# Kernel tuning notes

Measured on AMD Instinct MI355X. Metric: run time of the kernel, lower is better.

Reference implementation:

```python
import jax, jax.numpy as jnp
import numpy as np
from jax import lax

IMG_SIZE = 1024
NUM_CLASSES = 80
TOP_K = 300          # self.top_k
CLS_THRES = 0.05     # self.cls_thres
IOU_THR = 0.5        # nms overlap
BBOX_STD = jnp.array([0.1, 0.1, 0.2, 0.2], dtype=jnp.float32)


def make_anchors(img_size=IMG_SIZE):
    """Standard RetinaNet anchors: P3-P7, 3 ratios x 3 scales per cell."""
    strides = [8, 16, 32, 64, 128]
    ratios = np.array([0.5, 1.0, 2.0])
    scales = 2.0 ** (np.arange(3) / 3.0)
    out = []
    for s in strides:
        base = 4.0 * s
        ws, hs = [], []
        for r in ratios:
            for sc in scales:
                ws.append(base * sc / np.sqrt(r))
                hs.append(base * sc * np.sqrt(r))
        ws = np.array(ws); hs = np.array(hs)  # [9]
        fs = img_size // s
        shift = (np.arange(fs) + 0.5) * s
        cy, cx = np.meshgrid(shift, shift, indexing='ij')
        cx = cx.ravel()[:, None]; cy = cy.ravel()[:, None]
        a = np.stack([cx - ws / 2, cy - hs / 2, cx + ws / 2, cy + hs / 2], axis=-1)
        out.append(a.reshape(-1, 4))
    return np.concatenate(out, axis=0).astype(np.float32)  # [A,4]


def setup_inputs() -> dict:
    key = jax.random.key(0)
    k1, k2 = jax.random.split(key)
    anchors = jnp.asarray(make_anchors())[None]          # [1,A,4]
    A = anchors.shape[1]
    classifications = jax.random.uniform(k1, (1, A, NUM_CLASSES), dtype=jnp.float32)
    regressions = jax.random.normal(k2, (1, A, 4), dtype=jnp.float32)
    return {"classifications": classifications, "regressions": regressions,
            "anchors": anchors, "img_h": IMG_SIZE, "img_w": IMG_SIZE}


def decode_boxes(anchors, regressions):
    # BBoxTransform: mean=0, std=[.1,.1,.2,.2]
    w = anchors[..., 2] - anchors[..., 0]
    h = anchors[..., 3] - anchors[..., 1]
    cx = anchors[..., 0] + 0.5 * w
    cy = anchors[..., 1] + 0.5 * h
    d = regressions * BBOX_STD
    pcx = cx + d[..., 0] * w
    pcy = cy + d[..., 1] * h
    pw = jnp.exp(d[..., 2]) * w
    ph = jnp.exp(d[..., 3]) * h
    return jnp.stack([pcx - 0.5 * pw, pcy - 0.5 * ph,
                      pcx + 0.5 * pw, pcy + 0.5 * ph], axis=-1)


def pairwise_iou(b):  # b: [K,4]
    x1, y1, x2, y2 = b[:, 0], b[:, 1], b[:, 2], b[:, 3]
    area = jnp.clip(x2 - x1, 0) * jnp.clip(y2 - y1, 0)
    iw = jnp.clip(jnp.minimum(x2[:, None], x2[None]) - jnp.maximum(x1[:, None], x1[None]), 0)
    ih = jnp.clip(jnp.minimum(y2[:, None], y2[None]) - jnp.maximum(y1[:, None], y1[None]), 0)
    inter = iw * ih
    return inter / (area[:, None] + area[None] - inter + 1e-8)


def nms_one_class(boxes, scores_c):
    """Greedy NMS over top-K candidates above threshold for one class."""
    s = jnp.where(scores_c > CLS_THRES, scores_c, -jnp.inf)
    top_scores, top_idx = lax.top_k(s, TOP_K)        # sorted descending
    cand_valid = top_scores > CLS_THRES
    iou = pairwise_iou(boxes[top_idx])               # [K,K]
    idxs = jnp.arange(TOP_K)

    def body(suppressed, i):
        sup_i = suppressed[i] | (~cand_valid[i])
        new_sup = suppressed | ((~sup_i) & (iou[i] > IOU_THR) & (idxs > i))
        return new_sup, ~sup_i

    _, keep = lax.scan(body, jnp.zeros(TOP_K, bool), idxs)
    return top_idx, top_scores, keep


def reference(classifications, regressions, anchors, img_h, img_w):
    boxes = decode_boxes(anchors, regressions)       # [1,A,4]
    boxes = jnp.stack([jnp.maximum(boxes[..., 0], 0.0),
                       jnp.maximum(boxes[..., 1], 0.0),
                       jnp.minimum(boxes[..., 2], float(img_w)),
                       jnp.minimum(boxes[..., 3], float(img_h))], axis=-1)
    boxes0 = boxes[0]                                # [A,4]  (batch item 0, as original)
    cls0 = classifications[0]                        # [A,C]
    A, C = cls0.shape

    # per-class NMS, vmapped over the class axis
    top_idx, top_scores, keep = jax.vmap(nms_one_class, in_axes=(None, 1))(boxes0, cls0)
    # scatter kept scores back into dense [A,C] matrix (original 'scores' tensor)
    scores_mat = jnp.zeros((A, C), cls0.dtype).at[top_idx, jnp.arange(C)[:, None]].set(
        jnp.where(keep, top_scores, 0.0))

    scores_max = scores_mat.max(axis=1)
    labels = scores_mat.argmax(axis=1)
    valid = scores_max > 0
    # fixed-shape (jit-friendly) equivalent of the original's boolean filtering:
    final_scores = jnp.where(valid, scores_max, 0.0)
    final_labels = jnp.where(valid, labels, -1)
    final_boxes = jnp.where(valid[:, None], boxes0, 0.0)
    return final_scores, final_labels, final_boxes
```

## Files before the change

### kernel.cpp

```cpp
#include <hip/hip_runtime.h>
#include <cstdint>

typedef unsigned long long u64;
typedef unsigned int u32;

#define CLS_T    0.05f
#define T1G      0.997933f
#define TOPK     300
#define NWORDS   5
#define HBINS    2560
#define KEY_BASE 0x3D000000u
#define CCAP     512
#define NBLK     2048
#define SCAP     16
#define OVBIT    0x80000000u

__device__ inline u32 bin_of_bits(u32 bits) {
    u32 b = (bits - KEY_BASE) >> 14;
    if (b > (HBINS - 1)) b = HBINS - 1;
    return b;
}

__device__ inline float4 decode_box(const float* __restrict__ anc,
                                    const float* __restrict__ reg,
                                    u32 a, float W, float H)
{
    float x1 = anc[(size_t)a*4+0], y1 = anc[(size_t)a*4+1];
    float x2 = anc[(size_t)a*4+2], y2 = anc[(size_t)a*4+3];
    float w = x2 - x1, h = y2 - y1;
    float cx = x1 + 0.5f*w, cy = y1 + 0.5f*h;
    float r0 = reg[(size_t)a*4+0]*0.1f, r1 = reg[(size_t)a*4+1]*0.1f;
    float r2 = reg[(size_t)a*4+2]*0.2f, r3 = reg[(size_t)a*4+3]*0.2f;
    float pcx = cx + r0*w, pcy = cy + r1*h;
    float pw_ = expf(r2)*w, ph_ = expf(r3)*h;
    float4 b;
    b.x = fmaxf(pcx - 0.5f*pw_, 0.0f);
    b.y = fmaxf(pcy - 0.5f*ph_, 0.0f);
    b.z = fminf(pcx + 0.5f*pw_, W);
    b.w = fminf(pcy + 0.5f*ph_, H);
    return b;
}

__device__ inline void cex(u64& v, u64 p, bool lo, bool up) {
    u64 mx = v > p ? v : p;
    u64 mn = v > p ? p : v;
    v = (lo == up) ? mx : mn;
}
__device__ inline void s1(u64& v, u32 tid, u32 kk, u32 j) {
    u64 p = __shfl_xor((unsigned long long)v, (int)j, 64);
    cex(v, p, (tid & j) == 0, (tid & kk) == 0);
}
__device__ inline void l1(u64* sm, u64& v, u32 tid, u32 kk, u32 j) {
    __syncthreads();
    if (tid < 512) sm[tid] = v;
    __syncthreads();
    if (tid < 512) {
        u64 p = sm[tid ^ j];
        cex(v, p, (tid & j) == 0, (tid & kk) == 0);
    }
}

__global__ void decode_kernel(const float* __restrict__ anc,
                              const float* __restrict__ reg,
                              const int* __restrict__ ph,
                              const int* __restrict__ pw,
                              float* __restrict__ boxes,
                              u64* __restrict__ akey, int A)
{
    int a = blockIdx.x * blockDim.x + threadIdx.x;
    if (a >= A) return;
    akey[a] = 0;
    float W = (float)(*pw), H = (float)(*ph);
    float4 b = decode_box(anc, reg, (u32)a, W, H);
    boxes[a*4+0] = b.x; boxes[a*4+1] = b.y;
    boxes[a*4+2] = b.z; boxes[a*4+3] = b.w;
}

__global__ __launch_bounds__(256) void fused_scan_kernel(
    const float* __restrict__ cls,
    u64* __restrict__ akey,
    u64* __restrict__ gbuf, u32* __restrict__ segcnt, int A)
{
    const int tid = threadIdx.x;
    const int blk = blockIdx.x;

    for (int a = blk * 256 + tid; a < A; a += NBLK * 256) akey[a] = 0;

    __shared__ u32 cnt[80];
    __shared__ u64 buf[80][SCAP];
    __shared__ u32 s_over;
    for (int i = tid; i < 80; i += 256) cnt[i] = 0;
    if (tid == 0) s_over = 0;
    __syncthreads();

    size_t Nf4 = (size_t)A * 20;
    const size_t stride = (size_t)NBLK * 256;
    const float4* p4 = (const float4*)cls;
    for (size_t i = (size_t)blk * 256 + tid; i < Nf4; i += 2 * stride) {
        float4 v0 = p4[i];
        size_t i1 = i + stride;
        bool has1 = (i1 < Nf4);
        float4 v1;
        if (has1) v1 = p4[i1];
        {
            float ss[4] = {v0.x, v0.y, v0.z, v0.w};
            #pragma unroll
            for (int q = 0; q < 4; ++q) {
                if (ss[q] > T1G) {
                    u32 flat = (u32)(i * 4 + q);
                    u32 a = flat / 80u;
                    u32 c = flat - a * 80u;
                    u32 p = atomicAdd(&cnt[c], 1u);
                    if (p < SCAP) buf[c][p] = ((u64)__float_as_uint(ss[q]) << 32) | (u32)(~a);
                    else s_over = 1;
                }
            }
        }
        if (has1) {
            float ss[4] = {v1.x, v1.y, v1.z, v1.w};
            #pragma unroll
            for (int q = 0; q < 4; ++q) {
                if (ss[q] > T1G) {
                    u32 flat = (u32)(i1 * 4 + q);
                    u32 a = flat / 80u;
                    u32 c = flat - a * 80u;
                    u32 p = atomicAdd(&cnt[c], 1u);
                    if (p < SCAP) buf[c][p] = ((u64)__float_as_uint(ss[q]) << 32) | (u32)(~a);
                    else s_over = 1;
                }
            }
        }
    }
    __syncthreads();

    const u32 ob = s_over ? OVBIT : 0u;
    for (int m = tid; m < 80 * SCAP; m += 256) {
        int c = m / SCAP, e = m - c * SCAP;
        u32 cc = cnt[c]; if (cc > SCAP) cc = SCAP;
        if ((u32)e < cc)
            gbuf[((size_t)c * NBLK + blk) * SCAP + e] = buf[c][e];
    }
    for (int c = tid; c < 80; c += 256) {
        u32 cc = cnt[c]; if (cc > SCAP) cc = SCAP;
        segcnt[(size_t)c * NBLK + blk] = cc | ob;
    }
}

__global__ __launch_bounds__(640) void class_fused_kernel(
    const u32* __restrict__ segcnt, const u64* __restrict__ gbuf,
    const float* __restrict__ cls,
    const float* __restrict__ anc, const float* __restrict__ reg,
    const int* __restrict__ ph, const int* __restrict__ pw,
    u64* __restrict__ akey, int A, int C)
{
    const int c = blockIdx.x;
    const u32 tid = threadIdx.x;
    const int lane = tid & 63;

    __shared__ u32 sh[HBINS];
    __shared__ u32 sp[NBLK];
    __shared__ u64 cand[CCAP];
    __shared__ u32 wtot[8], wob[8];
    __shared__ u32 s_sel, s_cnt, s_rem;
    __shared__ float4 sbox[TOPK];
    __shared__ float  sbar[TOPK];
    __shared__ u64 iomaskT[NWORDS][TOPK];
    __shared__ u64 s_keep[NWORDS];

    const float W = (float)(*pw), H = (float)(*ph);

    u32 v4[4] = {0,0,0,0};
    u32 s = 0, ob = 0;
    if (tid < 512) {
        const u32* row = segcnt + (size_t)c * NBLK;
        #pragma unroll
        for (int q = 0; q < 4; ++q) {
            u32 r = row[tid * 4 + q];
            ob |= r & OVBIT;
            v4[q] = r & ~OVBIT;
            s += v4[q];
        }
    }
    u32 incl = s;
    #pragma unroll
    for (int d = 1; d < 64; d <<= 1) {
        u32 t = __shfl_up(incl, d, 64);
        if ((tid & 63) >= (u32)d) incl += t;
    }
    u64 obm = __ballot(ob != 0);
    if (tid < 512 && (tid & 63) == 63) {
        wtot[tid >> 6] = incl;
        wob [tid >> 6] = (obm != 0) ? 1u : 0u;
    }
    __syncthreads();
    u32 woff = 0, ntot = 0, obt = 0;
    #pragma unroll
    for (int w2 = 0; w2 < 8; ++w2) {
        u32 t = wtot[w2];
        obt |= wob[w2];
        if (w2 < (int)(tid >> 6)) woff += t;
        ntot += t;
    }
    if (tid < 512) {
        u32 base = woff + incl - s;
        #pragma unroll
        for (int q = 0; q < 4; ++q) { sp[tid * 4 + q] = base; base += v4[q]; }
    }
    __syncthreads();
    const u32 n = ntot;
    const bool over = (obt != 0);

    u32 cnt_f = 0;
    bool fast_ok = false;

    if (!over && n >= TOPK && n <= CCAP) {
        for (u32 i = tid; i < n; i += 640) {
            int lo = 0, hi = NBLK;
            while (hi - lo > 1) {
                int mid = (lo + hi) >> 1;
                if (sp[mid] <= i) lo = mid; else hi = mid;
            }
            u32 e = i - sp[lo];
            cand[i] = gbuf[((size_t)c * NBLK + lo) * SCAP + e];
        }
        cnt_f = n;
        fast_ok = true;
    }

    if (!fast_ok) {
        __syncthreads();
        for (int i = tid; i < HBINS; i += 640) sh[i] = 0;
        if (tid == 0) s_cnt = 0;
        __syncthreads();
        for (int a = tid; a < A; a += 640) {
            float sc = cls[(size_t)a * C + c];
            if (sc > CLS_T) atomicAdd(&sh[bin_of_bits(__float_as_uint(sc))], 1u);
        }
        __syncthreads();
        if (tid == 0) {
            u32 cum = 0; int sel = 0;
            for (int d = HBINS - 1; d >= 0; --d) {
                u32 nc = cum + sh[d];
                if (nc >= TOPK) { sel = d; break; }
                cum = nc;
            }
            s_sel = (u32)sel; s_rem = TOPK - cum;
        }
        __syncthreads();
        const u32 sel1 = s_sel;
        __syncthreads();
        for (int i = tid; i < 256; i += 640) sh[i] = 0;
        __syncthreads();
        for (int a = tid; a < A; a += 640) {
            float sc = cls[(size_t)a * C + c];
            if (sc > CLS_T) {
                u32 k = __float_as_uint(sc) - KEY_BASE;
                u32 b = k >> 14; if (b >= HBINS) b = HBINS - 1;
                if (b == sel1) atomicAdd(&sh[(k >> 6) & 0xFF], 1u);
            }
        }
        __syncthreads();
        if (tid == 0) {
            u32 rem = s_rem, cum = 0; int sel = 0;
            for (int d = 255; d >= 0; --d) {
                u32 nc = cum + sh[d];
                if (nc >= rem) { sel = d; break; }
                cum = nc;
            }
            s_sel = (sel1 << 14) | ((u32)sel << 6);
            s_cnt = 0;
        }
        __syncthreads();
        const u32 thresh = s_sel;
        for (int a = tid; a < A; a += 640) {
            float sc = cls[(size_t)a * C + c];
            if (sc > CLS_T) {
                u32 bits = __float_as_uint(sc);
                if (bits - KEY_BASE >= thresh) {
                    u32 p = atomicAdd(&s_cnt, 1u);
                    if (p < CCAP) cand[p] = ((u64)bits << 32) | (u32)(~(u32)a);
                }
            }
        }
        __syncthreads();
        cnt_f = s_cnt < CCAP ? s_cnt : CCAP;
    }

    for (u32 i = cnt_f + tid; i < CCAP; i += 640) cand[i] = 0;
    for (int m = tid; m < NWORDS * TOPK; m += 640) ((u64*)iomaskT)[m] = 0;
    __syncthreads();

    u64 v = 0;
    if (tid < 512) {
        v = cand[tid];
        for (u32 kk = 2; kk <= 64; kk <<= 1)
            for (u32 j = kk >> 1; j >= 1; j >>= 1)
                s1(v, tid, kk, j);
    }
    l1(cand, v, tid, 128u, 64u);
    if (tid < 512) for (u32 j = 32; j >= 1; j >>= 1) s1(v, tid, 128u, j);
    l1(cand, v, tid, 256u, 128u);
    l1(cand, v, tid, 256u, 64u);
    if (tid < 512) for (u32 j = 32; j >= 1; j >>= 1) s1(v, tid, 256u, j);
    l1(cand, v, tid, 512u, 256u);
    l1(cand, v, tid, 512u, 128u);
    l1(cand, v, tid, 512u, 64u);
    if (tid < 512) for (u32 j = 32; j >= 1; j >>= 1) s1(v, tid, 512u, j);

    const int T = (int)(cnt_f < TOPK ? cnt_f : TOPK);

    u64 key = v; u32 aidx = 0;
    if ((int)tid < T) {
        aidx = ~(u32)(key & 0xFFFFFFFFull);
        float4 b4 = decode_box(anc, reg, aidx, W, H);
        sbox[tid] = b4;
        sbar[tid] = fmaxf(b4.z - b4.x, 0.0f) * fmaxf(b4.w - b4.y, 0.0f);
    }
    __syncthreads();

    {
        const int jj = (int)(tid < 320 ? tid : tid - 320);
        const int p  = (int)(tid < 320 ? 0 : 1);
        if (jj < T) {
            float4 b = sbox[jj];
            float ar = sbar[jj];
            u64 cm[NWORDS] = {0,0,0,0,0};
            for (int i = p; i < jj; i += 2) {
                float4 bi = sbox[i];
                float iw = fmaxf(fminf(b.z, bi.z) - fmaxf(b.x, bi.x), 0.0f);
                float ih = fmaxf(fminf(b.w, bi.w) - fmaxf(b.y, bi.y), 0.0f);
                float inter = iw * ih;
                float uni = ((ar + sbar[i]) - inter) + 1e-8f;
                if (inter / uni > 0.5f) cm[i >> 6] |= 1ull << (i & 63);
            }
            #pragma unroll
            for (int w = 0; w < NWORDS; ++w)
                if (cm[w]) atomicOr(&iomaskT[w][jj], cm[w]);
        }
    }
    __syncthreads();

    if (tid < 64) {
        u64 K[NWORDS];
        #pragma unroll
        for (int w = 0; w < NWORDS; ++w) {
            int b = w * 64 + lane;
            bool valid = (b < T);
            u64 cmw = 0, se = 0;
            if (valid) {
                #pragma unroll
                for (int w2 = 0; w2 < NWORDS; ++w2)
                    if (w2 < w) se |= K[w2] & iomaskT[w2][b];
                cmw = iomaskT[w][b];
            }
            u64 U = __ballot(valid && se == 0);
            u64 Kw = 0;
            int guard = 0;
            while (U && guard++ < 64) {
                u64 newk = __ballot(((U >> lane) & 1ull) && ((cmw & U) == 0));
                Kw |= newk; U &= ~newk;
                u64 supp = __ballot((cmw & Kw) != 0);
                U &= ~supp;
            }
            K[w] = Kw;
        }
        if (lane == 0) {
            #pragma unroll
            for (int w = 0; w < NWORDS; ++w) s_keep[w] = K[w];
        }
    }
    __syncthreads();

    if ((int)tid < T) {
        if ((s_keep[tid >> 6] >> (tid & 63)) & 1ull) {
            u32 sbits = (u32)(key >> 32);
            u64 outk = ((u64)sbits << 32) | (u32)(255 - c);
            atomicMax(&akey[aidx], outk);
        }
    }
}

__global__ void finalize_kernel(const u64* __restrict__ akey,
                                const float* __restrict__ anc,
                                const float* __restrict__ reg,
                                const int* __restrict__ ph,
                                const int* __restrict__ pw,
                                float* __restrict__ out, int A)
{
    int a = blockIdx.x * blockDim.x + threadIdx.x;
    if (a >= A) return;
    float* scores = out;
    float* labels = out + A;
    float* boxes  = out + (size_t)2 * A;
    u64 k = akey[a];
    if (k) {
        scores[a] = __uint_as_float((u32)(k >> 32));
        labels[a] = (float)(int)(255u - (u32)(k & 0xFFFFFFFFull));
        float W = (float)(*pw), H = (float)(*ph);
        float4 b = decode_box(anc, reg, (u32)a, W, H);
        boxes[(size_t)a*4+0] = b.x; boxes[(size_t)a*4+1] = b.y;
        boxes[(size_t)a*4+2] = b.z; boxes[(size_t)a*4+3] = b.w;
    } else {
        scores[a] = 0.0f;
        labels[a] = -1.0f;
        boxes[(size_t)a*4+0] = 0.0f;
        boxes[(size_t)a*4+1] = 0.0f;
        boxes[(size_t)a*4+2] = 0.0f;
        boxes[(size_t)a*4+3] = 0.0f;
    }
}

__global__ void fb_finalize_kernel(const u64* __restrict__ akey,
                                   float* __restrict__ out, int A)
{
    int a = blockIdx.x * blockDim.x + threadIdx.x;
    if (a >= A) return;
    float* scores = out;
    float* labels = out + A;
    float* boxes  = out + (size_t)2 * A;
    u64 k = akey[a];
    if (k) {
        scores[a] = __uint_as_float((u32)(k >> 32));
        labels[a] = (float)(int)(255u - (u32)(k & 0xFFFFFFFFull));
    } else {
        scores[a] = 0.0f;
        labels[a] = -1.0f;
        boxes[(size_t)a*4+0] = 0.0f;
        boxes[(size_t)a*4+1] = 0.0f;
        boxes[(size_t)a*4+2] = 0.0f;
        boxes[(size_t)a*4+3] = 0.0f;
    }
}

#define FB_CAP 1024
__global__ __launch_bounds__(256) void fb_topk_nms_kernel(
    const float* __restrict__ cls,
    const float* __restrict__ boxes,
    u64* __restrict__ akey,
    int A, int C)
{
    const int c   = blockIdx.x;
    const int tid = threadIdx.x;

    __shared__ u32 hist[HBINS];
    __shared__ u64 cand[FB_CAP];
    __shared__ float bx1[TOPK], by1[TOPK], bx2[TOPK], by2[TOPK], bar[TOPK];
    __shared__ u64 iomask[TOPK][NWORDS];
    __shared__ u64 keepm[NWORDS];
    __shared__ u32 s_sel1, s_sel2, s_rem, s_cnt;

    for (int i = tid; i < HBINS; i += 256) hist[i] = 0;
    __syncthreads();
    for (int a = tid; a < A; a += 256) {
        float s = cls[(size_t)a * C + c];
        if (s > CLS_T) {
            u32 k = __float_as_uint(s) - KEY_BASE;
            u32 b = k >> 14; if (b >= HBINS) b = HBINS - 1;
            atomicAdd(&hist[b], 1u);
        }
    }
    __syncthreads();
    if (tid == 0) {
        u32 cum = 0; int sel = 0;
        for (int d = HBINS - 1; d >= 0; --d) {
            u32 nc = cum + hist[d];
            if (nc >= TOPK) { sel = d; break; }
            cum = nc;
        }
        s_sel1 = (u32)sel; s_rem = TOPK - cum;
    }
    __syncthreads();
    const u32 sel1 = s_sel1;

    for (int i = tid; i < 256; i += 256) hist[i] = 0;
    __syncthreads();
    for (int a = tid; a < A; a += 256) {
        float s = cls[(size_t)a * C + c];
        if (s > CLS_T) {
            u32 k = __float_as_uint(s) - KEY_BASE;
            u32 b = k >> 14; if (b >= HBINS) b = HBINS - 1;
            if (b == sel1) atomicAdd(&hist[(k >> 6) & 0xFF], 1u);
        }
    }
    __syncthreads();
    if (tid == 0) {
        u32 rem = s_rem, cum = 0; int sel = 0;
        for (int d = 255; d >= 0; --d) {
            u32 nc = cum + hist[d];
            if (nc >= rem) { sel = d; break; }
            cum = nc;
        }
        s_sel2 = (u32)sel; s_cnt = 0;
    }
    __syncthreads();
    const u32 thresh = (sel1 << 14) | (s_sel2 << 6);

    for (int a = tid; a < A; a += 256) {
        float s = cls[(size_t)a * C + c];
        if (s > CLS_T) {
            u32 bits = __float_as_uint(s);
            u32 k = bits - KEY_BASE;
            if (k >= thresh) {
                u32 pos = atomicAdd(&s_cnt, 1u);
                if (pos < FB_CAP) cand[pos] = ((u64)bits << 32) | (u32)(~(u32)a);
            }
        }
    }
    __syncthreads();
    const u32 total = s_cnt < FB_CAP ? s_cnt : FB_CAP;
    for (int i = tid; i < FB_CAP; i += 256)
        if (i >= (int)total) cand[i] = 0;
    __syncthreads();

    for (u32 kk = 2; kk <= FB_CAP; kk <<= 1) {
        for (u32 j = kk >> 1; j > 0; j >>= 1) {
            for (u32 i = tid; i < FB_CAP; i += 256) {
                u32 l = i ^ j;
                if (l > i) {
                    u64 av = cand[i], bv = cand[l];
                    bool up = ((i & kk) == 0);
                    if ((up && av < bv) || (!up && av > bv)) { cand[i] = bv; cand[l] = av; }
                }
            }
            __syncthreads();
        }
    }
    const int T = (int)(total < TOPK ? total : TOPK);

    for (int i = tid; i < T; i += 256) {
        u32 a = ~(u32)(cand[i] & 0xFFFFFFFFull);
        float x1 = boxes[(size_t)a*4+0], y1 = boxes[(size_t)a*4+1];
        float x2 = boxes[(size_t)a*4+2], y2 = boxes[(size_t)a*4+3];
        bx1[i] = x1; by1[i] = y1; bx2[i] = x2; by2[i] = y2;
        bar[i] = fmaxf(x2 - x1, 0.0f) * fmaxf(y2 - y1, 0.0f);
    }
    __syncthreads();

    for (int i = tid; i < T; i += 256) {
        u64 m[NWORDS] = {0,0,0,0,0};
        float x1 = bx1[i], y1 = by1[i], x2 = bx2[i], y2 = by2[i], ai = bar[i];
        for (int j = i + 1; j < T; ++j) {
            float iw = fmaxf(fminf(x2, bx2[j]) - fmaxf(x1, bx1[j]), 0.0f);
            float ih = fmaxf(fminf(y2, by2[j]) - fmaxf(y1, by1[j]), 0.0f);
            float inter = iw * ih;
            float uni = ((ai + bar[j]) - inter) + 1e-8f;
            if (inter / uni > 0.5f) m[j >> 6] |= 1ull << (j & 63);
        }
        for (int k2 = 0; k2 < NWORDS; ++k2) iomask[i][k2] = m[k2];
    }
    __syncthreads();

    if (tid == 0) {
        u64 sup[NWORDS] = {0,0,0,0,0};
        u64 kp [NWORDS] = {0,0,0,0,0};
        for (int i = 0; i < T; ++i) {
            if (!((sup[i >> 6] >> (i & 63)) & 1ull)) {
                kp[i >> 6] |= 1ull << (i & 63);
                for (int k2 = 0; k2 < NWORDS; ++k2) sup[k2] |= iomask[i][k2];
            }
        }
        for (int k2 = 0; k2 < NWORDS; ++k2) keepm[k2] = kp[k2];
    }
    __syncthreads();

    for (int i = tid; i < T; i += 256) {
        if ((keepm[i >> 6] >> (i & 63)) & 1ull) {
            u64 key = cand[i];
            u32 a = ~(u32)(key & 0xFFFFFFFFull);
            u32 sbits = (u32)(key >> 32);
            u64 outk = ((u64)sbits << 32) | (u32)(255 - c);
            atomicMax(&akey[a], outk);
        }
    }
}

extern "C" void kernel_launch(void* const* d_in, const int* in_sizes, int n_in,
                              void* d_out, int out_size, void* d_ws, size_t ws_size,
                              hipStream_t stream) {
    const float* cls = (const float*)d_in[0];
    const float* reg = (const float*)d_in[1];
    const float* anc = (const float*)d_in[2];
    const int*   ph  = (const int*)d_in[3];
    const int*   pw  = (const int*)d_in[4];

    int A = in_sizes[2] / 4;
    int C = in_sizes[0] / A;

    float* out       = (float*)d_out;
    float* out_boxes = out + (size_t)2 * A;

    size_t akey_bytes = (size_t)A * sizeof(u64);
    size_t off_sc     = (akey_bytes + 255) & ~(size_t)255;
    size_t sc_bytes   = (size_t)80 * NBLK * sizeof(u32);
    size_t off_gb     = (off_sc + sc_bytes + 255) & ~(size_t)255;
    size_t gb_bytes   = (size_t)80 * NBLK * SCAP * sizeof(u64);
    size_t need       = off_gb + gb_bytes;

    u64* akey = (u64*)d_ws;

    bool fastpath = (C == 80) && ((A & 3) == 0) && (A < (1 << 20)) && (ws_size >= need);

    if (fastpath) {
        u32* segcnt = (u32*)((char*)d_ws + off_sc);
        u64* gbuf   = (u64*)((char*)d_ws + off_gb);

        fused_scan_kernel<<<NBLK, 256, 0, stream>>>(cls, akey, gbuf, segcnt, A);
        class_fused_kernel<<<C, 640, 0, stream>>>(segcnt, gbuf, cls, anc, reg, ph, pw, akey, A, C);
        finalize_kernel<<<(A + 255) / 256, 256, 0, stream>>>(akey, anc, reg, ph, pw, out, A);
    } else {
        decode_kernel<<<(A + 255) / 256, 256, 0, stream>>>(anc, reg, ph, pw, out_boxes, akey, A);
        fb_topk_nms_kernel<<<C, 256, 0, stream>>>(cls, out_boxes, akey, A, C);
        fb_finalize_kernel<<<(A + 255) / 256, 256, 0, stream>>>(akey, out, A);
    }
}
```

Baseline: 52.21 us.

## Zero outputs in scan kernel and finalize only kept anchors via compact list

The output default fill (scores, labels, boxes) moves into the scan kernel's existing anchor loop. The class kernel now appends each kept anchor index to a global list through an atomic counter, and a light finalize kernel decodes boxes only for those entries instead of sweeping every anchor. Candidate gathering also changes from a per-element binary search to each thread copying its own segments directly. Duplicate anchors kept by several classes are written more than once with the same max key, and the direct copy adds serial per-thread loops.

```diff
diff --git a/kernel.cpp b/kernel.cpp
--- a/kernel.cpp
+++ b/kernel.cpp
@@ -14,6 +14,7 @@
 #define NBLK     2048
 #define SCAP     16
 #define OVBIT    0x80000000u
+#define KMAX     (80 * TOPK)
 
 __device__ inline u32 bin_of_bits(u32 bits) {
     u32 b = (bits - KEY_BASE) >> 14;
@@ -78,13 +79,25 @@
 
 __global__ __launch_bounds__(256) void fused_scan_kernel(
     const float* __restrict__ cls,
-    u64* __restrict__ akey,
-    u64* __restrict__ gbuf, u32* __restrict__ segcnt, int A)
+    u64* __restrict__ akey, float* __restrict__ out,
+    u64* __restrict__ gbuf, u32* __restrict__ segcnt,
+    u32* __restrict__ kcount, int A)
 {
     const int tid = threadIdx.x;
     const int blk = blockIdx.x;
 
-    for (int a = blk * 256 + tid; a < A; a += NBLK * 256) akey[a] = 0;
+    if (blk == 0 && tid == 0) *kcount = 0;
+
+    float* scores = out;
+    float* labels = out + A;
+    float4* boxes4 = (float4*)(out + (size_t)2 * A);
+    const float4 z4 = make_float4(0.f, 0.f, 0.f, 0.f);
+    for (int a = blk * 256 + tid; a < A; a += NBLK * 256) {
+        akey[a] = 0;
+        scores[a] = 0.0f;
+        labels[a] = -1.0f;
+        boxes4[a] = z4;
+    }
 
     __shared__ u32 cnt[80];
     __shared__ u64 buf[80][SCAP];
@@ -151,17 +164,17 @@
     const float* __restrict__ cls,
     const float* __restrict__ anc, const float* __restrict__ reg,
     const int* __restrict__ ph, const int* __restrict__ pw,
-    u64* __restrict__ akey, int A, int C)
+    u64* __restrict__ akey, u32* __restrict__ kcount, u32* __restrict__ klist,
+    int A, int C)
 {
     const int c = blockIdx.x;
     const u32 tid = threadIdx.x;
     const int lane = tid & 63;
 
     __shared__ u32 sh[HBINS];
-    __shared__ u32 sp[NBLK];
     __shared__ u64 cand[CCAP];
     __shared__ u32 wtot[8], wob[8];
-    __shared__ u32 s_sel, s_cnt, s_rem;
+    __shared__ u32 s_sel, s_cnt, s_rem, s_base;
     __shared__ float4 sbox[TOPK];
     __shared__ float  sbar[TOPK];
     __shared__ u64 iomaskT[NWORDS][TOPK];
@@ -201,12 +214,6 @@
         if (w2 < (int)(tid >> 6)) woff += t;
         ntot += t;
     }
-    if (tid < 512) {
-        u32 base = woff + incl - s;
-        #pragma unroll
-        for (int q = 0; q < 4; ++q) { sp[tid * 4 + q] = base; base += v4[q]; }
-    }
-    __syncthreads();
     const u32 n = ntot;
     const bool over = (obt != 0);
 
@@ -214,14 +221,14 @@
     bool fast_ok = false;
 
     if (!over && n >= TOPK && n <= CCAP) {
-        for (u32 i = tid; i < n; i += 640) {
-            int lo = 0, hi = NBLK;
-            while (hi - lo > 1) {
-                int mid = (lo + hi) >> 1;
-                if (sp[mid] <= i) lo = mid; else hi = mid;
-            }
-            u32 e = i - sp[lo];
-            cand[i] = gbuf[((size_t)c * NBLK + lo) * SCAP + e];
+        if (tid < 512) {
+            u32 base = woff + incl - s;
+            #pragma unroll
+            for (int q = 0; q < 4; ++q) {
+                const u64* src = gbuf + ((size_t)c * NBLK + tid * 4 + q) * SCAP;
+                for (u32 e = 0; e < v4[q]; ++e) cand[base + e] = src[e];
+                base += v4[q];
+            }
         }
         cnt_f = n;
         fast_ok = true;
@@ -371,43 +378,53 @@
     }
     __syncthreads();
 
+    if (tid == 0) {
+        u32 tot = 0;
+        #pragma unroll
+        for (int w = 0; w < NWORDS; ++w) tot += (u32)__popcll(s_keep[w]);
+        s_base = atomicAdd(kcount, tot);
+    }
+    __syncthreads();
+
     if ((int)tid < T) {
-        if ((s_keep[tid >> 6] >> (tid & 63)) & 1ull) {
+        int w = (int)(tid >> 6), b = (int)(tid & 63);
+        if ((s_keep[w] >> b) & 1ull) {
             u32 sbits = (u32)(key >> 32);
             u64 outk = ((u64)sbits << 32) | (u32)(255 - c);
             atomicMax(&akey[aidx], outk);
-        }
-    }
-}
-
-__global__ void finalize_kernel(const u64* __restrict__ akey,
-                                const float* __restrict__ anc,
-                                const float* __restrict__ reg,
-                                const int* __restrict__ ph,
-                                const int* __restrict__ pw,
-                                float* __restrict__ out, int A)
+            u32 rank = 0;
+            #pragma unroll
+            for (int w2 = 0; w2 < NWORDS; ++w2)
+                if (w2 < w) rank += (u32)__popcll(s_keep[w2]);
+            rank += (u32)__popcll(s_keep[w] & ((b == 0) ? 0ull : ((1ull << b) - 1ull)));
+            klist[s_base + rank] = aidx;
+        }
+    }
+}
+
+__global__ void finalize_lite_kernel(const u32* __restrict__ kcount,
+                                     const u32* __restrict__ klist,
+                                     const u64* __restrict__ akey,
+                                     const float* __restrict__ anc,
+                                     const float* __restrict__ reg,
+                                     const int* __restrict__ ph,
+                                     const int* __restrict__ pw,
+                                     float* __restrict__ out, int A)
 {
-    int a = blockIdx.x * blockDim.x + threadIdx.x;
-    if (a >= A) return;
+    u32 i = blockIdx.x * blockDim.x + threadIdx.x;
+    u32 kc = *kcount; if (kc > KMAX) kc = KMAX;
+    if (i >= kc) return;
+    u32 a = klist[i];
+    u64 k = akey[a];
     float* scores = out;
     float* labels = out + A;
     float* boxes  = out + (size_t)2 * A;
-    u64 k = akey[a];
-    if (k) {
-        scores[a] = __uint_as_float((u32)(k >> 32));
-        labels[a] = (float)(int)(255u - (u32)(k & 0xFFFFFFFFull));
-        float W = (float)(*pw), H = (float)(*ph);
-        float4 b = decode_box(anc, reg, (u32)a, W, H);
-        boxes[(size_t)a*4+0] = b.x; boxes[(size_t)a*4+1] = b.y;
-        boxes[(size_t)a*4+2] = b.z; boxes[(size_t)a*4+3] = b.w;
-    } else {
-        scores[a] = 0.0f;
-        labels[a] = -1.0f;
-        boxes[(size_t)a*4+0] = 0.0f;
-        boxes[(size_t)a*4+1] = 0.0f;
-        boxes[(size_t)a*4+2] = 0.0f;
-        boxes[(size_t)a*4+3] = 0.0f;
-    }
+    scores[a] = __uint_as_float((u32)(k >> 32));
+    labels[a] = (float)(int)(255u - (u32)(k & 0xFFFFFFFFull));
+    float W = (float)(*pw), H = (float)(*ph);
+    float4 b = decode_box(anc, reg, a, W, H);
+    boxes[(size_t)a*4+0] = b.x; boxes[(size_t)a*4+1] = b.y;
+    boxes[(size_t)a*4+2] = b.z; boxes[(size_t)a*4+3] = b.w;
 }
 
 __global__ void fb_finalize_kernel(const u64* __restrict__ akey,
@@ -590,7 +607,10 @@
     float* out_boxes = out + (size_t)2 * A;
 
     size_t akey_bytes = (size_t)A * sizeof(u64);
-    size_t off_sc     = (akey_bytes + 255) & ~(size_t)255;
+    size_t off_kc     = (akey_bytes + 255) & ~(size_t)255;
+    size_t off_kl     = (off_kc + 256 + 255) & ~(size_t)255;
+    size_t kl_bytes   = (size_t)KMAX * sizeof(u32);
+    size_t off_sc     = (off_kl + kl_bytes + 255) & ~(size_t)255;
     size_t sc_bytes   = (size_t)80 * NBLK * sizeof(u32);
     size_t off_gb     = (off_sc + sc_bytes + 255) & ~(size_t)255;
     size_t gb_bytes   = (size_t)80 * NBLK * SCAP * sizeof(u64);
@@ -601,12 +621,16 @@
     bool fastpath = (C == 80) && ((A & 3) == 0) && (A < (1 << 20)) && (ws_size >= need);
 
     if (fastpath) {
+        u32* kcount = (u32*)((char*)d_ws + off_kc);
+        u32* klist  = (u32*)((char*)d_ws + off_kl);
         u32* segcnt = (u32*)((char*)d_ws + off_sc);
         u64* gbuf   = (u64*)((char*)d_ws + off_gb);
 
-        fused_scan_kernel<<<NBLK, 256, 0, stream>>>(cls, akey, gbuf, segcnt, A);
-        class_fused_kernel<<<C, 640, 0, stream>>>(segcnt, gbuf, cls, anc, reg, ph, pw, akey, A, C);
-        finalize_kernel<<<(A + 255) / 256, 256, 0, stream>>>(akey, anc, reg, ph, pw, out, A);
+        fused_scan_kernel<<<NBLK, 256, 0, stream>>>(cls, akey, out, gbuf, segcnt, kcount, A);
+        class_fused_kernel<<<C, 640, 0, stream>>>(segcnt, gbuf, cls, anc, reg, ph, pw,
+                                                  akey, kcount, klist, A, C);
+        finalize_lite_kernel<<<(KMAX + 255) / 256, 256, 0, stream>>>(kcount, klist, akey,
+                                                                     anc, reg, ph, pw, out, A);
     } else {
         decode_kernel<<<(A + 255) / 256, 256, 0, stream>>>(anc, reg, ph, pw, out_boxes, akey, A);
         fb_topk_nms_kernel<<<C, 256, 0, stream>>>(cls, out_boxes, akey, A, C);
```

New measurement: 56.01 us. 7.3% more time.
